# Kernel optimization log

Measured on AMD Instinct MI355X. Metric: run time of the kernel, lower is better.

## Reference

```python
import math
import jax, jax.numpy as jnp
import numpy as np

H = 16  # num_heads

def get_alibi_slopes(n):
    def pow2_slopes(n):
        start = 2 ** (-2 ** (-(math.log2(n) - 3)))
        return [start * start ** i for i in range(n)]
    if math.log2(n).is_integer():
        return pow2_slopes(n)
    c = 2 ** math.floor(math.log2(n))
    return pow2_slopes(c) + get_alibi_slopes(2 * c)[0::2][: n - c]

def alibi_bias(num_heads, L, dtype=jnp.float32):
    slopes = jnp.asarray(get_alibi_slopes(num_heads), dtype=dtype)  # [H]
    pos = jnp.arange(L)
    rel = (pos[None, :] - pos[:, None]).astype(dtype)               # [L, L] = x - y
    bias = slopes[:, None, None] * rel[None, :, :]                  # [H, L, L]
    causal = pos[None, :] <= pos[:, None]                           # tril mask
    return jnp.where(causal[None, :, :], bias, -jnp.inf)


def setup_inputs() -> dict:
    key = jax.random.key(0)
    ks = jax.random.split(key, 4)
    D = 1024
    B, L = 2, 2048
    s_in = 1.0 / math.sqrt(D)
    return {
        "x": jax.random.normal(ks[0], (B, L, D), dtype=jnp.float32),
        "w_in": jax.random.normal(ks[1], (D, 3 * D), dtype=jnp.float32) * s_in,
        "b_in": jnp.zeros((3 * D,), dtype=jnp.float32),
        "w_out": jax.random.normal(ks[2], (D, D), dtype=jnp.float32) * s_in,
        "b_out": jnp.zeros((D,), dtype=jnp.float32),
    }


def reference(x, w_in, b_in, w_out, b_out):
    B, L, D = x.shape
    dh = D // H
    qkv = x @ w_in + b_in                                   # [B, L, 3D]
    q, k, v = jnp.split(qkv, 3, axis=-1)
    # [B, L, D] -> [B, H, L, dh]
    def heads(t):
        return t.reshape(B, L, H, dh).transpose(0, 2, 1, 3)
    q, k, v = heads(q), heads(k), heads(v)
    scores = jnp.einsum("bhqd,bhkd->bhqk", q, k) / math.sqrt(dh)
    scores = scores + alibi_bias(H, L, scores.dtype)[None]  # [B, H, L, L]
    attn = jax.nn.softmax(scores, axis=-1)
    out = jnp.einsum("bhqk,bhkd->bhqd", attn, v)            # [B, H, L, dh]
    out = out.transpose(0, 2, 1, 3).reshape(B, L, D)
    return out @ w_out + b_out
```

## Files before the change

### kernel.cpp

```cpp
#include <hip/hip_runtime.h>
#include <stdint.h>
#include <math.h>

#define NH 16
#define DH 64
#define SEQ 2048
#define DMODEL 1024

typedef short short8 __attribute__((ext_vector_type(8)));
typedef short short4v __attribute__((ext_vector_type(4)));
typedef float f32x4 __attribute__((ext_vector_type(4)));
typedef __bf16 bf16x4 __attribute__((ext_vector_type(4)));

__device__ __forceinline__ short f2bf(float f) {
  __bf16 h = (__bf16)f;
  return __builtin_bit_cast(short, h);
}
__device__ __forceinline__ short4v cvt4(f32x4 v) {
  bf16x4 b = __builtin_convertvector(v, bf16x4);
  return __builtin_bit_cast(short4v, b);
}
__device__ __forceinline__ float fast_exp2(float x) {
#if __has_builtin(__builtin_amdgcn_exp2f)
  return __builtin_amdgcn_exp2f(x);
#else
  return exp2f(x);
#endif
}

typedef const __attribute__((address_space(1))) uint32_t* gp_t;
typedef __attribute__((address_space(3))) uint32_t* lp_t;
__device__ __forceinline__ void async16(const short* g, short* l) {
  __builtin_amdgcn_global_load_lds((gp_t)g, (lp_t)l, 16, 0, 0);
}

__device__ __forceinline__ void transpose_tile(const float* __restrict__ in,
                                               short* __restrict__ out, int R, int C,
                                               int t, int tilesX, int tid) {
  __shared__ float tile[32][33];
  const int tx = tid & 31, ty = tid >> 5;
  const int c0 = (t % tilesX) * 32, r0 = (t / tilesX) * 32;
#pragma unroll
  for (int i = 0; i < 4; ++i)
    tile[ty + i * 8][tx] = in[(size_t)(r0 + ty + i * 8) * C + c0 + tx];
  __syncthreads();
#pragma unroll
  for (int i = 0; i < 4; ++i)
    out[(size_t)(c0 + ty + i * 8) * R + r0 + tx] = f2bf(tile[tx][ty + i * 8]);
}

__global__ void k_prep(const float* __restrict__ x, short* __restrict__ xb,
                       const float* __restrict__ w_in, short* __restrict__ w_in_t,
                       const float* __restrict__ w_out, short* __restrict__ w_out_t) {
  const int tid = threadIdx.x;
  const int blk = blockIdx.x;
  if (blk < 4096) {
    const int i = blk * 256 + tid;
    f32x4 v = ((const f32x4*)x)[i];
    ((short4v*)xb)[i] = cvt4(v);
  } else if (blk < 4096 + 3072) {
    transpose_tile(w_in, w_in_t, 1024, 3072, blk - 4096, 96, tid);
  } else {
    transpose_tile(w_out, w_out_t, 1024, 1024, blk - 7168, 32, tid);
  }
}

template <int MODE>
__launch_bounds__(256, 3)
__global__ void k_gemm(const short* __restrict__ A, const short* __restrict__ Bt,
                       const float* __restrict__ bias, float* __restrict__ Cf,
                       short* __restrict__ qo, short* __restrict__ ko,
                       short* __restrict__ vo) {
  constexpr int KD = 1024;
  __shared__ __align__(16) short As[128 * 64];
  __shared__ __align__(16) short Bs[128 * 64];
  const int tid = threadIdx.x;
  const int wave = tid >> 6, lane = tid & 63;
  const int quad = lane >> 4, l16 = lane & 15;
  const int wm = wave >> 1, wn = wave & 1;
  const int tM = blockIdx.y * 128, tN = blockIdx.x * 128;

  const short* pA[4];
  const short* pB[4];
  short* lA[4];
  short* lB[4];
#pragma unroll
  for (int t = 0; t < 4; ++t) {
    const int c = t * 256 + tid;
    const int row = c >> 3, gch = (c & 7) ^ (row & 7);
    pA[t] = A + (size_t)(tM + row) * KD + gch * 8;
    pB[t] = Bt + (size_t)(tN + row) * KD + gch * 8;
    lA[t] = &As[c * 8];
    lB[t] = &Bs[c * 8];
  }

  const int sw = l16 & 7;
  const int col0 = (quad ^ sw) << 3;
  const int col1 = col0 ^ 32;

  f32x4 acc[4][4] = {};

  for (int k0 = 0; k0 < KD; k0 += 64) {
    __syncthreads();
#pragma unroll
    for (int t = 0; t < 4; ++t) {
      async16(pA[t] + k0, lA[t]);
      async16(pB[t] + k0, lB[t]);
    }
    __syncthreads();
#pragma unroll
    for (int kh = 0; kh < 2; ++kh) {
      const int col = kh ? col1 : col0;
      short8 af[4], bfr[4];
#pragma unroll
      for (int i = 0; i < 4; ++i)
        af[i] = *(const short8*)&As[(wm * 64 + i * 16 + l16) * 64 + col];
#pragma unroll
      for (int i = 0; i < 4; ++i)
        bfr[i] = *(const short8*)&Bs[(wn * 64 + i * 16 + l16) * 64 + col];
#pragma unroll
      for (int i = 0; i < 4; ++i)
#pragma unroll
        for (int j = 0; j < 4; ++j)
          acc[i][j] = __builtin_amdgcn_mfma_f32_16x16x32_bf16(af[i], bfr[j], acc[i][j], 0, 0, 0);
    }
  }

  const int rbase = tM + wm * 64 + quad * 4;
#pragma unroll
  for (int i = 0; i < 4; ++i) {
#pragma unroll
    for (int j = 0; j < 4; ++j) {
      const int col = tN + wn * 64 + j * 16 + l16;
      const float bi = bias[col];
      if (MODE == 0) {
        const int which = col >> 10;
        const int h = (col & 1023) >> 6, d = col & 63;
        if (which == 2) {
          const int row0 = rbase + i * 16;
          const int b = row0 >> 11, li0 = row0 & 2047;
          f32x4 t;
#pragma unroll
          for (int rr = 0; rr < 4; ++rr) t[rr] = acc[i][j][rr] + bi;
          *(short4v*)&vo[(((size_t)(b * NH + h)) * DH + d) * SEQ + li0] = cvt4(t);
        } else {
          short* dst = (which == 0) ? qo : ko;
#pragma unroll
          for (int rr = 0; rr < 4; ++rr) {
            const int row = rbase + i * 16 + rr;
            const int b = row >> 11, li = row & 2047;
            dst[(((size_t)(b * NH + h)) * SEQ + li) * DH + d] = f2bf(acc[i][j][rr] + bi);
          }
        }
      } else {
#pragma unroll
        for (int rr = 0; rr < 4; ++rr) {
          const int row = rbase + i * 16 + rr;
          Cf[(size_t)row * DMODEL + col] = acc[i][j][rr] + bi;
        }
      }
    }
  }
}

__launch_bounds__(256)
__global__ void k_attn(const short* __restrict__ q, const short* __restrict__ k,
                       const short* __restrict__ vt, short* __restrict__ o) {
  __shared__ __align__(16) short Ks[2][64 * 64];
  __shared__ __align__(16) short Vs[2][64 * 64];
  __shared__ __align__(16) short Ps[4][16 * 64];
  const int tid = threadIdx.x;
  const int wave = tid >> 6, lane = tid & 63;
  const int quad = lane >> 4, l16 = lane & 15;
  const int sw = l16 & 7;
  const int bx = blockIdx.x;
  const int g = bx >> 5, g0 = g & 7, sel = g >> 3;
  const int qt = (sel == 0) ? 31 - g0 : (sel == 1) ? g0 : (sel == 2) ? 23 - g0 : 8 + g0;
  const int bh = bx & 31;
  const int h = bh & (NH - 1);
  const size_t base = (size_t)bh * SEQ * DH;
  const float LOG2E = 1.44269504088896f;
  const float slope2 = exp2f(-0.5f * (float)(h + 1)) * LOG2E;
  const float scale2 = 0.125f * LOG2E;
  const float FM = 12.0f;

  const int c0i = tid, c1i = 256 + tid;
  const int r0 = c0i >> 3, ch0 = (c0i & 7) ^ (r0 & 7);
  const int r1 = c1i >> 3, ch1 = (c1i & 7) ^ (r1 & 7);
  const int qk_off0 = r0 * DH + ch0 * 8;
  const int qk_off1 = r1 * DH + ch1 * 8;
  const int v_off0 = r0 * SEQ + ch0 * 8;
  const int v_off1 = r1 * SEQ + ch1 * 8;

  const int col0 = ((quad ^ sw) << 3);
  const int col1 = col0 ^ 32;
  int psoff[4];
#pragma unroll
  for (int in = 0; in < 4; ++in)
    psoff[in] = l16 * 64 + (((2 * in + (quad >> 1)) ^ sw) << 3) + (quad & 1) * 4;
  const int qlim4 = wave * 16 + l16 - 4 * quad;

  const int q0 = qt * 64;
  const int qrow = q0 + wave * 16 + l16;
  const short* qp = q + base + (size_t)qrow * DH + quad * 8;
  const short8 qb0 = *(const short8*)qp;
  const short8 qb1 = *(const short8*)(qp + 32);

  short8 ones;
#pragma unroll
  for (int j = 0; j < 8; ++j) ones[j] = (short)0x3F80;

  f32x4 accO[4] = {};
  f32x4 accL = {};
  const float qoff = -slope2 * (float)qrow - FM + slope2 * (float)(4 * quad);
  float inoff[4];
#pragma unroll
  for (int in = 0; in < 4; ++in)
    inoff[in] = qoff + slope2 * (float)(16 * in);
  const float s64 = slope2 * 64.0f;
  float rc[4];
#pragma unroll
  for (int r = 0; r < 4; ++r) rc[r] = slope2 * (float)r;

  const short* kp = k + base;
  const short* vp = vt + base;

  async16(kp + qk_off0, &Ks[0][c0i * 8]);
  async16(kp + qk_off1, &Ks[0][c1i * 8]);
  async16(vp + v_off0, &Vs[0][c0i * 8]);
  async16(vp + v_off1, &Vs[0][c1i * 8]);
  kp += 64 * DH;
  vp += 64;
  __syncthreads();

  short8 paA, paB;
  short8 var0[4], var1[4];

  for (int kt = 0; kt <= qt; ++kt) {
    const int cur = kt & 1, nxt = cur ^ 1;
    if (kt < qt) {
      async16(kp + qk_off0, &Ks[nxt][c0i * 8]);
      async16(kp + qk_off1, &Ks[nxt][c1i * 8]);
      async16(vp + v_off0, &Vs[nxt][c0i * 8]);
      async16(vp + v_off1, &Vs[nxt][c1i * 8]);
      kp += 64 * DH;
      vp += 64;
    }

    f32x4 s[4];
    __builtin_amdgcn_s_setprio(1);
#pragma unroll
    for (int in = 0; in < 4; ++in) {
      const short8 ka0 = *(const short8*)&Ks[cur][(in * 16 + l16) * 64 + col0];
      const short8 ka1 = *(const short8*)&Ks[cur][(in * 16 + l16) * 64 + col1];
      f32x4 t = {};
      t = __builtin_amdgcn_mfma_f32_16x16x32_bf16(ka0, qb0, t, 0, 0, 0);
      t = __builtin_amdgcn_mfma_f32_16x16x32_bf16(ka1, qb1, t, 0, 0, 0);
      s[in] = t;
    }

    if (kt > 0) {
      accL = __builtin_amdgcn_mfma_f32_16x16x32_bf16(ones, paA, accL, 0, 0, 0);
      accL = __builtin_amdgcn_mfma_f32_16x16x32_bf16(ones, paB, accL, 0, 0, 0);
#pragma unroll
      for (int i = 0; i < 4; ++i) {
        accO[i] = __builtin_amdgcn_mfma_f32_16x16x32_bf16(var0[i], paA, accO[i], 0, 0, 0);
        accO[i] = __builtin_amdgcn_mfma_f32_16x16x32_bf16(var1[i], paB, accO[i], 0, 0, 0);
      }
    }
    __builtin_amdgcn_s_setprio(0);

#pragma unroll
    for (int i = 0; i < 4; ++i) {
      var0[i] = *(const short8*)&Vs[cur][(i * 16 + l16) * 64 + col0];
      var1[i] = *(const short8*)&Vs[cur][(i * 16 + l16) * 64 + col1];
    }

    if (kt == qt) {
#pragma unroll
      for (int in = 0; in < 4; ++in) {
        f32x4 p;
#pragma unroll
        for (int r = 0; r < 4; ++r) {
          float val = fast_exp2(fmaf(s[in][r], scale2, inoff[in] + rc[r]));
          p[r] = (16 * in + r <= qlim4) ? val : 0.f;
        }
        *(short4v*)&Ps[wave][psoff[in]] = cvt4(p);
      }
    } else {
#pragma unroll
      for (int in = 0; in < 4; ++in) {
        f32x4 p;
#pragma unroll
        for (int r = 0; r < 4; ++r)
          p[r] = fast_exp2(fmaf(s[in][r], scale2, inoff[in] + rc[r]));
        *(short4v*)&Ps[wave][psoff[in]] = cvt4(p);
      }
    }
#pragma unroll
    for (int in = 0; in < 4; ++in) inoff[in] += s64;

    paA = *(const short8*)&Ps[wave][l16 * 64 + col0];
    paB = *(const short8*)&Ps[wave][l16 * 64 + col1];

    __syncthreads();
  }

  __builtin_amdgcn_s_setprio(1);
  accL = __builtin_amdgcn_mfma_f32_16x16x32_bf16(ones, paA, accL, 0, 0, 0);
  accL = __builtin_amdgcn_mfma_f32_16x16x32_bf16(ones, paB, accL, 0, 0, 0);
#pragma unroll
  for (int i = 0; i < 4; ++i) {
    accO[i] = __builtin_amdgcn_mfma_f32_16x16x32_bf16(var0[i], paA, accO[i], 0, 0, 0);
    accO[i] = __builtin_amdgcn_mfma_f32_16x16x32_bf16(var1[i], paB, accO[i], 0, 0, 0);
  }
  __builtin_amdgcn_s_setprio(0);

  const float inv = 1.0f / accL[0];
  const int b = bh >> 4;
  short* ob = o + ((((size_t)b * SEQ + qrow) * NH + h) * DH + 4 * quad);
#pragma unroll
  for (int i = 0; i < 4; ++i) {
    f32x4 t;
#pragma unroll
    for (int r = 0; r < 4; ++r) t[r] = accO[i][r] * inv;
    *(short4v*)&ob[16 * i] = cvt4(t);
  }
}

extern "C" void kernel_launch(void* const* d_in, const int* in_sizes, int n_in,
                              void* d_out, int out_size, void* d_ws, size_t ws_size,
                              hipStream_t stream) {
  const float* x = (const float*)d_in[0];
  const float* w_in = (const float*)d_in[1];
  const float* b_in = (const float*)d_in[2];
  const float* w_out = (const float*)d_in[3];
  const float* b_out = (const float*)d_in[4];
  float* out = (float*)d_out;

  char* ws = (char*)d_ws;
  short* xb = (short*)(ws);
  short* w_in_t = (short*)(ws + (8u << 20));
  short* w_out_t = (short*)(ws + (14u << 20));
  short* qv = (short*)(ws + (16u << 20));
  short* kv = (short*)(ws + (24u << 20));
  short* vv = (short*)(ws + (32u << 20));
  short* ao = (short*)(ws + (40u << 20));

  k_prep<<<8192, 256, 0, stream>>>(x, xb, w_in, w_in_t, w_out, w_out_t);
  k_gemm<0><<<dim3(24, 32), 256, 0, stream>>>(xb, w_in_t, b_in, nullptr, qv, kv, vv);
  k_attn<<<1024, 256, 0, stream>>>(qv, kv, vv, ao);
  k_gemm<1><<<dim3(8, 32), 256, 0, stream>>>(ao, w_out_t, b_out, out, nullptr, nullptr, nullptr);
}
```

Baseline: 167.4 us.

## Split attention waves 2x2 over query and key halves with cross-wave reduction

Each wave now handles 32 query rows against half of the 64-key tile (2x2 wave grid) instead of 16 query rows against the full tile. Each K fragment is reused for two query blocks, and each V fragment read is halved. The row-sum MFMA with a ones vector is replaced by scalar accumulation of the probabilities plus a shuffle reduction. Partial outputs from the two key-half waves are combined through shared memory at the end, which adds an extra sync and LDS traffic and changes register pressure.

```diff
diff --git a/kernel.cpp b/kernel.cpp
--- a/kernel.cpp
+++ b/kernel.cpp
@@ -173,6 +173,7 @@
   const int wave = tid >> 6, lane = tid & 63;
   const int quad = lane >> 4, l16 = lane & 15;
   const int sw = l16 & 7;
+  const int qh = wave >> 1, kh = wave & 1;
   const int bx = blockIdx.x;
   const int g = bx >> 5, g0 = g & 7, sel = g >> 3;
   const int qt = (sel == 0) ? 31 - g0 : (sel == 1) ? g0 : (sel == 2) ? 23 - g0 : 8 + g0;
@@ -192,35 +193,49 @@
   const int v_off0 = r0 * SEQ + ch0 * 8;
   const int v_off1 = r1 * SEQ + ch1 * 8;
 
-  const int col0 = ((quad ^ sw) << 3);
-  const int col1 = col0 ^ 32;
-  int psoff[4];
-#pragma unroll
-  for (int in = 0; in < 4; ++in)
-    psoff[in] = l16 * 64 + (((2 * in + (quad >> 1)) ^ sw) << 3) + (quad & 1) * 4;
-  const int qlim4 = wave * 16 + l16 - 4 * quad;
-
   const int q0 = qt * 64;
-  const int qrow = q0 + wave * 16 + l16;
-  const short* qp = q + base + (size_t)qrow * DH + quad * 8;
-  const short8 qb0 = *(const short8*)qp;
-  const short8 qb1 = *(const short8*)(qp + 32);
-
-  short8 ones;
-#pragma unroll
-  for (int j = 0; j < 8; ++j) ones[j] = (short)0x3F80;
-
-  f32x4 accO[4] = {};
-  f32x4 accL = {};
-  const float qoff = -slope2 * (float)qrow - FM + slope2 * (float)(4 * quad);
-  float inoff[4];
-#pragma unroll
-  for (int in = 0; in < 4; ++in)
-    inoff[in] = qoff + slope2 * (float)(16 * in);
+  const int qrowA = q0 + qh * 32 + l16;
+  const int qrowB = qrowA + 16;
+
+  const short* qpA = q + base + (size_t)qrowA * DH + quad * 8;
+  const short* qpB = q + base + (size_t)qrowB * DH + quad * 8;
+  const short8 qA0 = *(const short8*)qpA;
+  const short8 qA1 = *(const short8*)(qpA + 32);
+  const short8 qB0 = *(const short8*)qpB;
+  const short8 qB1 = *(const short8*)(qpB + 32);
+
+  const int kcol0 = (quad ^ sw) << 3;
+  const int kcol1 = kcol0 ^ 32;
+  const int vcol = (((kh * 4 + quad) ^ sw) << 3);
+  int pwoff[2][2];
+#pragma unroll
+  for (int qb = 0; qb < 2; ++qb)
+#pragma unroll
+    for (int kb = 0; kb < 2; ++kb)
+      pwoff[qb][kb] = l16 * 64 + ((((qb * 4 + kb * 2 + (quad >> 1))) ^ sw) << 3) + (quad & 1) * 4;
+  const int proff0 = l16 * 64 + (((0 * 4 + quad) ^ sw) << 3);
+  const int proff1 = l16 * 64 + (((1 * 4 + quad) ^ sw) << 3);
+
+  float ioff[2][2];
+#pragma unroll
+  for (int qb = 0; qb < 2; ++qb)
+#pragma unroll
+    for (int kb = 0; kb < 2; ++kb)
+      ioff[qb][kb] = -slope2 * (float)(q0 + qh * 32 + qb * 16 + l16) - FM +
+                     slope2 * (float)(kh * 32 + kb * 16 + 4 * quad);
   const float s64 = slope2 * 64.0f;
   float rc[4];
 #pragma unroll
   for (int r = 0; r < 4; ++r) rc[r] = slope2 * (float)r;
+  int lim[2][2];
+#pragma unroll
+  for (int qb = 0; qb < 2; ++qb)
+#pragma unroll
+    for (int kb = 0; kb < 2; ++kb)
+      lim[qb][kb] = (qh - kh) * 32 + 16 * (qb - kb) + l16 - 4 * quad;
+
+  f32x4 accO[4][2] = {};
+  float accLp[2] = {0.f, 0.f};
 
   const short* kp = k + base;
   const short* vp = vt + base;
@@ -234,7 +249,7 @@
   __syncthreads();
 
   short8 paA, paB;
-  short8 var0[4], var1[4];
+  short8 var[4];
 
   for (int kt = 0; kt <= qt; ++kt) {
     const int cur = kt & 1, nxt = cur ^ 1;
@@ -247,84 +262,121 @@
       vp += 64;
     }
 
-    f32x4 s[4];
+    f32x4 s[2][2];
     __builtin_amdgcn_s_setprio(1);
 #pragma unroll
-    for (int in = 0; in < 4; ++in) {
-      const short8 ka0 = *(const short8*)&Ks[cur][(in * 16 + l16) * 64 + col0];
-      const short8 ka1 = *(const short8*)&Ks[cur][(in * 16 + l16) * 64 + col1];
-      f32x4 t = {};
-      t = __builtin_amdgcn_mfma_f32_16x16x32_bf16(ka0, qb0, t, 0, 0, 0);
-      t = __builtin_amdgcn_mfma_f32_16x16x32_bf16(ka1, qb1, t, 0, 0, 0);
-      s[in] = t;
+    for (int kb = 0; kb < 2; ++kb) {
+      const int in = 2 * kh + kb;
+      const short8 ka0 = *(const short8*)&Ks[cur][(in * 16 + l16) * 64 + kcol0];
+      const short8 ka1 = *(const short8*)&Ks[cur][(in * 16 + l16) * 64 + kcol1];
+      f32x4 t0 = {};
+      t0 = __builtin_amdgcn_mfma_f32_16x16x32_bf16(ka0, qA0, t0, 0, 0, 0);
+      t0 = __builtin_amdgcn_mfma_f32_16x16x32_bf16(ka1, qA1, t0, 0, 0, 0);
+      s[kb][0] = t0;
+      f32x4 t1 = {};
+      t1 = __builtin_amdgcn_mfma_f32_16x16x32_bf16(ka0, qB0, t1, 0, 0, 0);
+      t1 = __builtin_amdgcn_mfma_f32_16x16x32_bf16(ka1, qB1, t1, 0, 0, 0);
+      s[kb][1] = t1;
     }
 
     if (kt > 0) {
-      accL = __builtin_amdgcn_mfma_f32_16x16x32_bf16(ones, paA, accL, 0, 0, 0);
-      accL = __builtin_amdgcn_mfma_f32_16x16x32_bf16(ones, paB, accL, 0, 0, 0);
 #pragma unroll
       for (int i = 0; i < 4; ++i) {
-        accO[i] = __builtin_amdgcn_mfma_f32_16x16x32_bf16(var0[i], paA, accO[i], 0, 0, 0);
-        accO[i] = __builtin_amdgcn_mfma_f32_16x16x32_bf16(var1[i], paB, accO[i], 0, 0, 0);
+        accO[i][0] = __builtin_amdgcn_mfma_f32_16x16x32_bf16(var[i], paA, accO[i][0], 0, 0, 0);
+        accO[i][1] = __builtin_amdgcn_mfma_f32_16x16x32_bf16(var[i], paB, accO[i][1], 0, 0, 0);
       }
     }
     __builtin_amdgcn_s_setprio(0);
 
 #pragma unroll
-    for (int i = 0; i < 4; ++i) {
-      var0[i] = *(const short8*)&Vs[cur][(i * 16 + l16) * 64 + col0];
-      var1[i] = *(const short8*)&Vs[cur][(i * 16 + l16) * 64 + col1];
-    }
+    for (int i = 0; i < 4; ++i)
+      var[i] = *(const short8*)&Vs[cur][(i * 16 + l16) * 64 + vcol];
 
     if (kt == qt) {
 #pragma unroll
-      for (int in = 0; in < 4; ++in) {
-        f32x4 p;
-#pragma unroll
-        for (int r = 0; r < 4; ++r) {
-          float val = fast_exp2(fmaf(s[in][r], scale2, inoff[in] + rc[r]));
-          p[r] = (16 * in + r <= qlim4) ? val : 0.f;
+      for (int kb = 0; kb < 2; ++kb)
+#pragma unroll
+        for (int qb = 0; qb < 2; ++qb) {
+          f32x4 p;
+#pragma unroll
+          for (int r = 0; r < 4; ++r) {
+            float val = fast_exp2(fmaf(s[kb][qb][r], scale2, ioff[qb][kb] + rc[r]));
+            p[r] = (r <= lim[qb][kb]) ? val : 0.f;
+          }
+          accLp[qb] += p[0] + p[1] + p[2] + p[3];
+          *(short4v*)&Ps[wave][pwoff[qb][kb]] = cvt4(p);
         }
-        *(short4v*)&Ps[wave][psoff[in]] = cvt4(p);
+    } else {
+#pragma unroll
+      for (int kb = 0; kb < 2; ++kb)
+#pragma unroll
+        for (int qb = 0; qb < 2; ++qb) {
+          f32x4 p;
+#pragma unroll
+          for (int r = 0; r < 4; ++r)
+            p[r] = fast_exp2(fmaf(s[kb][qb][r], scale2, ioff[qb][kb] + rc[r]));
+          accLp[qb] += p[0] + p[1] + p[2] + p[3];
+          *(short4v*)&Ps[wave][pwoff[qb][kb]] = cvt4(p);
+        }
+    }
+#pragma unroll
+    for (int qb = 0; qb < 2; ++qb)
+#pragma unroll
+      for (int kb = 0; kb < 2; ++kb) ioff[qb][kb] += s64;
+
+    paA = *(const short8*)&Ps[wave][proff0];
+    paB = *(const short8*)&Ps[wave][proff1];
+
+    __syncthreads();
+  }
+
+#pragma unroll
+  for (int i = 0; i < 4; ++i) {
+    accO[i][0] = __builtin_amdgcn_mfma_f32_16x16x32_bf16(var[i], paA, accO[i][0], 0, 0, 0);
+    accO[i][1] = __builtin_amdgcn_mfma_f32_16x16x32_bf16(var[i], paB, accO[i][1], 0, 0, 0);
+  }
+
+  __syncthreads();
+  float* scr = (qh == 0) ? (float*)&Ks[0][0] : (float*)&Vs[0][0];
+  float* s0 = scr + lane * 40;
+  if (kh) {
+#pragma unroll
+    for (int i = 0; i < 4; ++i)
+#pragma unroll
+      for (int qb = 0; qb < 2; ++qb)
+        *(f32x4*)&s0[(i * 2 + qb) * 4] = accO[i][qb];
+    s0[32] = accLp[0];
+    s0[33] = accLp[1];
+  }
+  __syncthreads();
+  if (!kh) {
+#pragma unroll
+    for (int i = 0; i < 4; ++i)
+#pragma unroll
+      for (int qb = 0; qb < 2; ++qb) {
+        f32x4 t = *(const f32x4*)&s0[(i * 2 + qb) * 4];
+#pragma unroll
+        for (int r = 0; r < 4; ++r) accO[i][qb][r] += t[r];
       }
-    } else {
-#pragma unroll
-      for (int in = 0; in < 4; ++in) {
-        f32x4 p;
-#pragma unroll
-        for (int r = 0; r < 4; ++r)
-          p[r] = fast_exp2(fmaf(s[in][r], scale2, inoff[in] + rc[r]));
-        *(short4v*)&Ps[wave][psoff[in]] = cvt4(p);
+    accLp[0] += s0[32];
+    accLp[1] += s0[33];
+    const int b = bh >> 4;
+#pragma unroll
+    for (int qb = 0; qb < 2; ++qb) {
+      float lsum = accLp[qb];
+      lsum += __shfl_xor(lsum, 16);
+      lsum += __shfl_xor(lsum, 32);
+      const float inv = 1.0f / lsum;
+      const int qrow = (qb == 0) ? qrowA : qrowB;
+      short* ob = o + ((((size_t)b * SEQ + qrow) * NH + h) * DH + 4 * quad);
+#pragma unroll
+      for (int i = 0; i < 4; ++i) {
+        f32x4 t;
+#pragma unroll
+        for (int r = 0; r < 4; ++r) t[r] = accO[i][qb][r] * inv;
+        *(short4v*)&ob[16 * i] = cvt4(t);
       }
     }
-#pragma unroll
-    for (int in = 0; in < 4; ++in) inoff[in] += s64;
-
-    paA = *(const short8*)&Ps[wave][l16 * 64 + col0];
-    paB = *(const short8*)&Ps[wave][l16 * 64 + col1];
-
-    __syncthreads();
-  }
-
-  __builtin_amdgcn_s_setprio(1);
-  accL = __builtin_amdgcn_mfma_f32_16x16x32_bf16(ones, paA, accL, 0, 0, 0);
-  accL = __builtin_amdgcn_mfma_f32_16x16x32_bf16(ones, paB, accL, 0, 0, 0);
-#pragma unroll
-  for (int i = 0; i < 4; ++i) {
-    accO[i] = __builtin_amdgcn_mfma_f32_16x16x32_bf16(var0[i], paA, accO[i], 0, 0, 0);
-    accO[i] = __builtin_amdgcn_mfma_f32_16x16x32_bf16(var1[i], paB, accO[i], 0, 0, 0);
-  }
-  __builtin_amdgcn_s_setprio(0);
-
-  const float inv = 1.0f / accL[0];
-  const int b = bh >> 4;
-  short* ob = o + ((((size_t)b * SEQ + qrow) * NH + h) * DH + 4 * quad);
-#pragma unroll
-  for (int i = 0; i < 4; ++i) {
-    f32x4 t;
-#pragma unroll
-    for (int r = 0; r < 4; ++r) t[r] = accO[i][r] * inv;
-    *(short4v*)&ob[16 * i] = cvt4(t);
   }
 }
 
```

Result: slower. 183.5 us (+9.6%).

## Pair complementary causal query tiles per attention block for balanced work

Applied to the files above, without the earlier changes.

Each attention block now processes two query tiles, qt=31-g and qt=g, one after the other. Every block therefore does a constant 33 key-tile iterations, and the grid shrinks from 1024 to 512 blocks. The K/V prefetch for the second tile is issued during the last iteration of the first, so the pipeline keeps running across the boundary. The aim is to remove causal load imbalance and tail effects. The cost is fewer blocks available for latency hiding, plus the s_setprio hint dropped from the epilogue.

```diff
diff --git a/kernel.cpp b/kernel.cpp
--- a/kernel.cpp
+++ b/kernel.cpp
@@ -174,9 +174,9 @@
   const int quad = lane >> 4, l16 = lane & 15;
   const int sw = l16 & 7;
   const int bx = blockIdx.x;
-  const int g = bx >> 5, g0 = g & 7, sel = g >> 3;
-  const int qt = (sel == 0) ? 31 - g0 : (sel == 1) ? g0 : (sel == 2) ? 23 - g0 : 8 + g0;
+  const int g = bx >> 5;
   const int bh = bx & 31;
+  const int qtA = 31 - g, qtB = g;
   const int h = bh & (NH - 1);
   const size_t base = (size_t)bh * SEQ * DH;
   const float LOG2E = 1.44269504088896f;
@@ -200,27 +200,15 @@
     psoff[in] = l16 * 64 + (((2 * in + (quad >> 1)) ^ sw) << 3) + (quad & 1) * 4;
   const int qlim4 = wave * 16 + l16 - 4 * quad;
 
-  const int q0 = qt * 64;
-  const int qrow = q0 + wave * 16 + l16;
-  const short* qp = q + base + (size_t)qrow * DH + quad * 8;
-  const short8 qb0 = *(const short8*)qp;
-  const short8 qb1 = *(const short8*)(qp + 32);
-
   short8 ones;
 #pragma unroll
   for (int j = 0; j < 8; ++j) ones[j] = (short)0x3F80;
 
-  f32x4 accO[4] = {};
-  f32x4 accL = {};
-  const float qoff = -slope2 * (float)qrow - FM + slope2 * (float)(4 * quad);
-  float inoff[4];
-#pragma unroll
-  for (int in = 0; in < 4; ++in)
-    inoff[in] = qoff + slope2 * (float)(16 * in);
   const float s64 = slope2 * 64.0f;
   float rc[4];
 #pragma unroll
   for (int r = 0; r < 4; ++r) rc[r] = slope2 * (float)r;
+  const int b = bh >> 4;
 
   const short* kp = k + base;
   const short* vp = vt + base;
@@ -236,95 +224,202 @@
   short8 paA, paB;
   short8 var0[4], var1[4];
 
-  for (int kt = 0; kt <= qt; ++kt) {
-    const int cur = kt & 1, nxt = cur ^ 1;
-    if (kt < qt) {
+  {
+    const int qrow = qtA * 64 + wave * 16 + l16;
+    const short* qp = q + base + (size_t)qrow * DH + quad * 8;
+    const short8 qb0 = *(const short8*)qp;
+    const short8 qb1 = *(const short8*)(qp + 32);
+    float inoff[4];
+    const float qoff = -slope2 * (float)qrow - FM + slope2 * (float)(4 * quad);
+#pragma unroll
+    for (int in = 0; in < 4; ++in) inoff[in] = qoff + slope2 * (float)(16 * in);
+    f32x4 accO[4] = {};
+    f32x4 accL = {};
+
+    for (int kt = 0; kt <= qtA; ++kt) {
+      const int cur = kt & 1, nxt = cur ^ 1;
+      if (kt == qtA) { kp = k + base; vp = vt + base; }
       async16(kp + qk_off0, &Ks[nxt][c0i * 8]);
       async16(kp + qk_off1, &Ks[nxt][c1i * 8]);
       async16(vp + v_off0, &Vs[nxt][c0i * 8]);
       async16(vp + v_off1, &Vs[nxt][c1i * 8]);
       kp += 64 * DH;
       vp += 64;
-    }
-
-    f32x4 s[4];
-    __builtin_amdgcn_s_setprio(1);
-#pragma unroll
-    for (int in = 0; in < 4; ++in) {
-      const short8 ka0 = *(const short8*)&Ks[cur][(in * 16 + l16) * 64 + col0];
-      const short8 ka1 = *(const short8*)&Ks[cur][(in * 16 + l16) * 64 + col1];
-      f32x4 t = {};
-      t = __builtin_amdgcn_mfma_f32_16x16x32_bf16(ka0, qb0, t, 0, 0, 0);
-      t = __builtin_amdgcn_mfma_f32_16x16x32_bf16(ka1, qb1, t, 0, 0, 0);
-      s[in] = t;
-    }
-
-    if (kt > 0) {
-      accL = __builtin_amdgcn_mfma_f32_16x16x32_bf16(ones, paA, accL, 0, 0, 0);
-      accL = __builtin_amdgcn_mfma_f32_16x16x32_bf16(ones, paB, accL, 0, 0, 0);
+
+      f32x4 s[4];
+      __builtin_amdgcn_s_setprio(1);
+#pragma unroll
+      for (int in = 0; in < 4; ++in) {
+        const short8 ka0 = *(const short8*)&Ks[cur][(in * 16 + l16) * 64 + col0];
+        const short8 ka1 = *(const short8*)&Ks[cur][(in * 16 + l16) * 64 + col1];
+        f32x4 t = {};
+        t = __builtin_amdgcn_mfma_f32_16x16x32_bf16(ka0, qb0, t, 0, 0, 0);
+        t = __builtin_amdgcn_mfma_f32_16x16x32_bf16(ka1, qb1, t, 0, 0, 0);
+        s[in] = t;
+      }
+      if (kt > 0) {
+        accL = __builtin_amdgcn_mfma_f32_16x16x32_bf16(ones, paA, accL, 0, 0, 0);
+        accL = __builtin_amdgcn_mfma_f32_16x16x32_bf16(ones, paB, accL, 0, 0, 0);
+#pragma unroll
+        for (int i = 0; i < 4; ++i) {
+          accO[i] = __builtin_amdgcn_mfma_f32_16x16x32_bf16(var0[i], paA, accO[i], 0, 0, 0);
+          accO[i] = __builtin_amdgcn_mfma_f32_16x16x32_bf16(var1[i], paB, accO[i], 0, 0, 0);
+        }
+      }
+      __builtin_amdgcn_s_setprio(0);
+
 #pragma unroll
       for (int i = 0; i < 4; ++i) {
-        accO[i] = __builtin_amdgcn_mfma_f32_16x16x32_bf16(var0[i], paA, accO[i], 0, 0, 0);
-        accO[i] = __builtin_amdgcn_mfma_f32_16x16x32_bf16(var1[i], paB, accO[i], 0, 0, 0);
-      }
-    }
-    __builtin_amdgcn_s_setprio(0);
-
+        var0[i] = *(const short8*)&Vs[cur][(i * 16 + l16) * 64 + col0];
+        var1[i] = *(const short8*)&Vs[cur][(i * 16 + l16) * 64 + col1];
+      }
+
+      if (kt == qtA) {
+#pragma unroll
+        for (int in = 0; in < 4; ++in) {
+          f32x4 p;
+#pragma unroll
+          for (int r = 0; r < 4; ++r) {
+            float val = fast_exp2(fmaf(s[in][r], scale2, inoff[in] + rc[r]));
+            p[r] = (16 * in + r <= qlim4) ? val : 0.f;
+          }
+          *(short4v*)&Ps[wave][psoff[in]] = cvt4(p);
+        }
+      } else {
+#pragma unroll
+        for (int in = 0; in < 4; ++in) {
+          f32x4 p;
+#pragma unroll
+          for (int r = 0; r < 4; ++r)
+            p[r] = fast_exp2(fmaf(s[in][r], scale2, inoff[in] + rc[r]));
+          *(short4v*)&Ps[wave][psoff[in]] = cvt4(p);
+        }
+      }
+#pragma unroll
+      for (int in = 0; in < 4; ++in) inoff[in] += s64;
+
+      paA = *(const short8*)&Ps[wave][l16 * 64 + col0];
+      paB = *(const short8*)&Ps[wave][l16 * 64 + col1];
+
+      __syncthreads();
+    }
+
+    accL = __builtin_amdgcn_mfma_f32_16x16x32_bf16(ones, paA, accL, 0, 0, 0);
+    accL = __builtin_amdgcn_mfma_f32_16x16x32_bf16(ones, paB, accL, 0, 0, 0);
 #pragma unroll
     for (int i = 0; i < 4; ++i) {
-      var0[i] = *(const short8*)&Vs[cur][(i * 16 + l16) * 64 + col0];
-      var1[i] = *(const short8*)&Vs[cur][(i * 16 + l16) * 64 + col1];
-    }
-
-    if (kt == qt) {
+      accO[i] = __builtin_amdgcn_mfma_f32_16x16x32_bf16(var0[i], paA, accO[i], 0, 0, 0);
+      accO[i] = __builtin_amdgcn_mfma_f32_16x16x32_bf16(var1[i], paB, accO[i], 0, 0, 0);
+    }
+    const float inv = 1.0f / accL[0];
+    short* ob = o + ((((size_t)b * SEQ + qrow) * NH + h) * DH + 4 * quad);
+#pragma unroll
+    for (int i = 0; i < 4; ++i) {
+      f32x4 t;
+#pragma unroll
+      for (int r = 0; r < 4; ++r) t[r] = accO[i][r] * inv;
+      *(short4v*)&ob[16 * i] = cvt4(t);
+    }
+  }
+
+  {
+    const int qrow = qtB * 64 + wave * 16 + l16;
+    const short* qp = q + base + (size_t)qrow * DH + quad * 8;
+    const short8 qb0 = *(const short8*)qp;
+    const short8 qb1 = *(const short8*)(qp + 32);
+    float inoff[4];
+    const float qoff = -slope2 * (float)qrow - FM + slope2 * (float)(4 * quad);
+#pragma unroll
+    for (int in = 0; in < 4; ++in) inoff[in] = qoff + slope2 * (float)(16 * in);
+    f32x4 accO[4] = {};
+    f32x4 accL = {};
+    const int par = (qtA + 1) & 1;
+
+    for (int kt = 0; kt <= qtB; ++kt) {
+      const int cur = (par + kt) & 1, nxt = cur ^ 1;
+      if (kt < qtB) {
+        async16(kp + qk_off0, &Ks[nxt][c0i * 8]);
+        async16(kp + qk_off1, &Ks[nxt][c1i * 8]);
+        async16(vp + v_off0, &Vs[nxt][c0i * 8]);
+        async16(vp + v_off1, &Vs[nxt][c1i * 8]);
+        kp += 64 * DH;
+        vp += 64;
+      }
+
+      f32x4 s[4];
+      __builtin_amdgcn_s_setprio(1);
 #pragma unroll
       for (int in = 0; in < 4; ++in) {
-        f32x4 p;
-#pragma unroll
-        for (int r = 0; r < 4; ++r) {
-          float val = fast_exp2(fmaf(s[in][r], scale2, inoff[in] + rc[r]));
-          p[r] = (16 * in + r <= qlim4) ? val : 0.f;
-        }
-        *(short4v*)&Ps[wave][psoff[in]] = cvt4(p);
-      }
-    } else {
-#pragma unroll
-      for (int in = 0; in < 4; ++in) {
-        f32x4 p;
-#pragma unroll
-        for (int r = 0; r < 4; ++r)
-          p[r] = fast_exp2(fmaf(s[in][r], scale2, inoff[in] + rc[r]));
-        *(short4v*)&Ps[wave][psoff[in]] = cvt4(p);
-      }
-    }
-#pragma unroll
-    for (int in = 0; in < 4; ++in) inoff[in] += s64;
-
-    paA = *(const short8*)&Ps[wave][l16 * 64 + col0];
-    paB = *(const short8*)&Ps[wave][l16 * 64 + col1];
-
-    __syncthreads();
-  }
-
-  __builtin_amdgcn_s_setprio(1);
-  accL = __builtin_amdgcn_mfma_f32_16x16x32_bf16(ones, paA, accL, 0, 0, 0);
-  accL = __builtin_amdgcn_mfma_f32_16x16x32_bf16(ones, paB, accL, 0, 0, 0);
-#pragma unroll
-  for (int i = 0; i < 4; ++i) {
-    accO[i] = __builtin_amdgcn_mfma_f32_16x16x32_bf16(var0[i], paA, accO[i], 0, 0, 0);
-    accO[i] = __builtin_amdgcn_mfma_f32_16x16x32_bf16(var1[i], paB, accO[i], 0, 0, 0);
-  }
-  __builtin_amdgcn_s_setprio(0);
-
-  const float inv = 1.0f / accL[0];
-  const int b = bh >> 4;
-  short* ob = o + ((((size_t)b * SEQ + qrow) * NH + h) * DH + 4 * quad);
-#pragma unroll
-  for (int i = 0; i < 4; ++i) {
-    f32x4 t;
-#pragma unroll
-    for (int r = 0; r < 4; ++r) t[r] = accO[i][r] * inv;
-    *(short4v*)&ob[16 * i] = cvt4(t);
+        const short8 ka0 = *(const short8*)&Ks[cur][(in * 16 + l16) * 64 + col0];
+        const short8 ka1 = *(const short8*)&Ks[cur][(in * 16 + l16) * 64 + col1];
+        f32x4 t = {};
+        t = __builtin_amdgcn_mfma_f32_16x16x32_bf16(ka0, qb0, t, 0, 0, 0);
+        t = __builtin_amdgcn_mfma_f32_16x16x32_bf16(ka1, qb1, t, 0, 0, 0);
+        s[in] = t;
+      }
+      if (kt > 0) {
+        accL = __builtin_amdgcn_mfma_f32_16x16x32_bf16(ones, paA, accL, 0, 0, 0);
+        accL = __builtin_amdgcn_mfma_f32_16x16x32_bf16(ones, paB, accL, 0, 0, 0);
+#pragma unroll
+        for (int i = 0; i < 4; ++i) {
+          accO[i] = __builtin_amdgcn_mfma_f32_16x16x32_bf16(var0[i], paA, accO[i], 0, 0, 0);
+          accO[i] = __builtin_amdgcn_mfma_f32_16x16x32_bf16(var1[i], paB, accO[i], 0, 0, 0);
+        }
+      }
+      __builtin_amdgcn_s_setprio(0);
+
+#pragma unroll
+      for (int i = 0; i < 4; ++i) {
+        var0[i] = *(const short8*)&Vs[cur][(i * 16 + l16) * 64 + col0];
+        var1[i] = *(const short8*)&Vs[cur][(i * 16 + l16) * 64 + col1];
+      }
+
+      if (kt == qtB) {
+#pragma unroll
+        for (int in = 0; in < 4; ++in) {
+          f32x4 p;
+#pragma unroll
+          for (int r = 0; r < 4; ++r) {
+            float val = fast_exp2(fmaf(s[in][r], scale2, inoff[in] + rc[r]));
+            p[r] = (16 * in + r <= qlim4) ? val : 0.f;
+          }
+          *(short4v*)&Ps[wave][psoff[in]] = cvt4(p);
+        }
+      } else {
+#pragma unroll
+        for (int in = 0; in < 4; ++in) {
+          f32x4 p;
+#pragma unroll
+          for (int r = 0; r < 4; ++r)
+            p[r] = fast_exp2(fmaf(s[in][r], scale2, inoff[in] + rc[r]));
+          *(short4v*)&Ps[wave][psoff[in]] = cvt4(p);
+        }
+      }
+#pragma unroll
+      for (int in = 0; in < 4; ++in) inoff[in] += s64;
+
+      paA = *(const short8*)&Ps[wave][l16 * 64 + col0];
+      paB = *(const short8*)&Ps[wave][l16 * 64 + col1];
+
+      __syncthreads();
+    }
+
+    accL = __builtin_amdgcn_mfma_f32_16x16x32_bf16(ones, paA, accL, 0, 0, 0);
+    accL = __builtin_amdgcn_mfma_f32_16x16x32_bf16(ones, paB, accL, 0, 0, 0);
+#pragma unroll
+    for (int i = 0; i < 4; ++i) {
+      accO[i] = __builtin_amdgcn_mfma_f32_16x16x32_bf16(var0[i], paA, accO[i], 0, 0, 0);
+      accO[i] = __builtin_amdgcn_mfma_f32_16x16x32_bf16(var1[i], paB, accO[i], 0, 0, 0);
+    }
+    const float inv = 1.0f / accL[0];
+    short* ob = o + ((((size_t)b * SEQ + qrow) * NH + h) * DH + 4 * quad);
+#pragma unroll
+    for (int i = 0; i < 4; ++i) {
+      f32x4 t;
+#pragma unroll
+      for (int r = 0; r < 4; ++r) t[r] = accO[i][r] * inv;
+      *(short4v*)&ob[16 * i] = cvt4(t);
+    }
   }
 }
 
@@ -349,6 +444,6 @@
 
   k_prep<<<8192, 256, 0, stream>>>(x, xb, w_in, w_in_t, w_out, w_out_t);
   k_gemm<0><<<dim3(24, 32), 256, 0, stream>>>(xb, w_in_t, b_in, nullptr, qv, kv, vv);
-  k_attn<<<1024, 256, 0, stream>>>(qv, kv, vv, ao);
+  k_attn<<<512, 256, 0, stream>>>(qv, kv, vv, ao);
   k_gemm<1><<<dim3(8, 32), 256, 0, stream>>>(ao, w_out_t, b_out, out, nullptr, nullptr, nullptr);
 }
```

Result: slower. 176.3 us (+5.3%).

## Split long causal attention tiles across KV halves with separate normalize kernel

Applied to the files above, without the earlier changes.

The attention kernel now splits query tiles 16-31 into two blocks, each covering half of the key range, so the grid grows from 1024 to 1536 blocks with more even work per block. Each block writes unnormalized fp32 output and row sums to a workspace, and a new k_norm kernel adds the partial results, divides by the summed denominator and writes bf16. This relies on the fixed exponent offset (no running max), so partial sums can be added directly. It adds an extra launch and the fp32 partial writes and reads, in exchange for better load balance and shorter tail blocks.

```diff
diff --git a/kernel.cpp b/kernel.cpp
--- a/kernel.cpp
+++ b/kernel.cpp
@@ -165,7 +165,7 @@
 
 __launch_bounds__(256)
 __global__ void k_attn(const short* __restrict__ q, const short* __restrict__ k,
-                       const short* __restrict__ vt, short* __restrict__ o) {
+                       const short* __restrict__ vt, float* __restrict__ po) {
   __shared__ __align__(16) short Ks[2][64 * 64];
   __shared__ __align__(16) short Vs[2][64 * 64];
   __shared__ __align__(16) short Ps[4][16 * 64];
@@ -174,9 +174,16 @@
   const int quad = lane >> 4, l16 = lane & 15;
   const int sw = l16 & 7;
   const int bx = blockIdx.x;
-  const int g = bx >> 5, g0 = g & 7, sel = g >> 3;
-  const int qt = (sel == 0) ? 31 - g0 : (sel == 1) ? g0 : (sel == 2) ? 23 - g0 : 8 + g0;
-  const int bh = bx & 31;
+  const int sb = bx >> 5, bh = bx & 31;
+  int qt, k0t, k1t;
+  if (sb < 32) {
+    qt = 31 - (sb >> 1);
+    const int h0 = (qt + 1) >> 1;
+    if (sb & 1) { k0t = h0; k1t = qt + 1; } else { k0t = 0; k1t = h0; }
+  } else {
+    qt = 47 - sb;
+    k0t = 0; k1t = qt + 1;
+  }
   const int h = bh & (NH - 1);
   const size_t base = (size_t)bh * SEQ * DH;
   const float LOG2E = 1.44269504088896f;
@@ -212,18 +219,17 @@
 
   f32x4 accO[4] = {};
   f32x4 accL = {};
-  const float qoff = -slope2 * (float)qrow - FM + slope2 * (float)(4 * quad);
   float inoff[4];
 #pragma unroll
   for (int in = 0; in < 4; ++in)
-    inoff[in] = qoff + slope2 * (float)(16 * in);
+    inoff[in] = slope2 * (float)(64 * k0t + 16 * in + 4 * quad - qrow) - FM;
   const float s64 = slope2 * 64.0f;
   float rc[4];
 #pragma unroll
   for (int r = 0; r < 4; ++r) rc[r] = slope2 * (float)r;
 
-  const short* kp = k + base;
-  const short* vp = vt + base;
+  const short* kp = k + base + (size_t)k0t * 64 * DH;
+  const short* vp = vt + base + (size_t)k0t * 64;
 
   async16(kp + qk_off0, &Ks[0][c0i * 8]);
   async16(kp + qk_off1, &Ks[0][c1i * 8]);
@@ -236,9 +242,10 @@
   short8 paA, paB;
   short8 var0[4], var1[4];
 
-  for (int kt = 0; kt <= qt; ++kt) {
-    const int cur = kt & 1, nxt = cur ^ 1;
-    if (kt < qt) {
+  for (int kt = k0t; kt < k1t; ++kt) {
+    const int t = kt - k0t;
+    const int cur = t & 1, nxt = cur ^ 1;
+    if (kt + 1 < k1t) {
       async16(kp + qk_off0, &Ks[nxt][c0i * 8]);
       async16(kp + qk_off1, &Ks[nxt][c1i * 8]);
       async16(vp + v_off0, &Vs[nxt][c0i * 8]);
@@ -253,13 +260,13 @@
     for (int in = 0; in < 4; ++in) {
       const short8 ka0 = *(const short8*)&Ks[cur][(in * 16 + l16) * 64 + col0];
       const short8 ka1 = *(const short8*)&Ks[cur][(in * 16 + l16) * 64 + col1];
-      f32x4 t = {};
-      t = __builtin_amdgcn_mfma_f32_16x16x32_bf16(ka0, qb0, t, 0, 0, 0);
-      t = __builtin_amdgcn_mfma_f32_16x16x32_bf16(ka1, qb1, t, 0, 0, 0);
-      s[in] = t;
-    }
-
-    if (kt > 0) {
+      f32x4 t2 = {};
+      t2 = __builtin_amdgcn_mfma_f32_16x16x32_bf16(ka0, qb0, t2, 0, 0, 0);
+      t2 = __builtin_amdgcn_mfma_f32_16x16x32_bf16(ka1, qb1, t2, 0, 0, 0);
+      s[in] = t2;
+    }
+
+    if (t > 0) {
       accL = __builtin_amdgcn_mfma_f32_16x16x32_bf16(ones, paA, accL, 0, 0, 0);
       accL = __builtin_amdgcn_mfma_f32_16x16x32_bf16(ones, paB, accL, 0, 0, 0);
 #pragma unroll
@@ -316,15 +323,47 @@
   }
   __builtin_amdgcn_s_setprio(0);
 
-  const float inv = 1.0f / accL[0];
-  const int b = bh >> 4;
-  short* ob = o + ((((size_t)b * SEQ + qrow) * NH + h) * DH + 4 * quad);
-#pragma unroll
-  for (int i = 0; i < 4; ++i) {
+  float* ps = po + (size_t)bx * 4160;
+  const int prow = wave * 16 + l16;
+#pragma unroll
+  for (int i = 0; i < 4; ++i)
+    *(f32x4*)&ps[prow * 64 + i * 16 + 4 * quad] = accO[i];
+  if (quad == 0) ps[4096 + prow] = accL[0];
+}
+
+__launch_bounds__(256)
+__global__ void k_norm(const float* __restrict__ po, short* __restrict__ ao) {
+  const int p = blockIdx.x;
+  const int bh = p & 31, qt = p >> 5;
+  const int tid = threadIdx.x;
+  const int row = tid >> 2, c0 = (tid & 3) * 16;
+  const float* s0;
+  const float* s1 = nullptr;
+  if (qt >= 16) {
+    const int sb0 = 2 * (31 - qt);
+    s0 = po + (size_t)(sb0 * 32 + bh) * 4160;
+    s1 = po + (size_t)((sb0 + 1) * 32 + bh) * 4160;
+  } else {
+    s0 = po + (size_t)((47 - qt) * 32 + bh) * 4160;
+  }
+  float L = s0[4096 + row];
+  if (s1) L += s1[4096 + row];
+  const float inv = 1.0f / L;
+  const int b = bh >> 4, h = bh & 15;
+  const int qrow = qt * 64 + row;
+  short* ob = ao + (((size_t)b * SEQ + qrow) * NH + h) * DH + c0;
+#pragma unroll
+  for (int j = 0; j < 4; ++j) {
+    f32x4 v = *(const f32x4*)&s0[row * 64 + c0 + j * 4];
+    if (s1) {
+      f32x4 w = *(const f32x4*)&s1[row * 64 + c0 + j * 4];
+#pragma unroll
+      for (int r = 0; r < 4; ++r) v[r] += w[r];
+    }
     f32x4 t;
 #pragma unroll
-    for (int r = 0; r < 4; ++r) t[r] = accO[i][r] * inv;
-    *(short4v*)&ob[16 * i] = cvt4(t);
+    for (int r = 0; r < 4; ++r) t[r] = v[r] * inv;
+    *(short4v*)&ob[j * 4] = cvt4(t);
   }
 }
 
@@ -346,9 +385,11 @@
   short* kv = (short*)(ws + (24u << 20));
   short* vv = (short*)(ws + (32u << 20));
   short* ao = (short*)(ws + (40u << 20));
+  float* po = (float*)(ws + (48u << 20));
 
   k_prep<<<8192, 256, 0, stream>>>(x, xb, w_in, w_in_t, w_out, w_out_t);
   k_gemm<0><<<dim3(24, 32), 256, 0, stream>>>(xb, w_in_t, b_in, nullptr, qv, kv, vv);
-  k_attn<<<1024, 256, 0, stream>>>(qv, kv, vv, ao);
+  k_attn<<<1536, 256, 0, stream>>>(qv, kv, vv, po);
+  k_norm<<<1024, 256, 0, stream>>>(po, ao);
   k_gemm<1><<<dim3(8, 32), 256, 0, stream>>>(ao, w_out_t, b_out, out, nullptr, nullptr, nullptr);
 }
```

Measured after the change: 183.6 us. 1.1x slower.
